# Optimization experiments

Measured on AMD Instinct MI355X. Metric: run time of the kernel, lower is better.

The kernel has to match this reference:

```python
import jax, jax.numpy as jnp
import numpy as np

B, C1, C2, D, NH, H, W = 2, 64, 256, 256, 8, 64, 64
HD = D // NH
EPS = 1e-5


def setup_inputs() -> dict:
    key = jax.random.key(0)
    ks = jax.random.split(key, 12)
    s = lambda fan_in: 1.0 / np.sqrt(fan_in)
    return {
        "F_lidar": jax.random.normal(ks[0], (B, C1, H, W), jnp.float32),
        "F_cam": jax.random.normal(ks[1], (B, C2, H, W), jnp.float32),
        "Wq": jax.random.normal(ks[2], (D, C1), jnp.float32) * s(C1),
        "Wk": jax.random.normal(ks[3], (D, C2), jnp.float32) * s(C2),
        "Wv": jax.random.normal(ks[4], (D, C2), jnp.float32) * s(C2),
        "Wo": jax.random.normal(ks[5], (D, D), jnp.float32) * s(D),
        "Wres": jax.random.normal(ks[6], (D, C1), jnp.float32) * s(C1),
        "g1": jnp.ones((D,), jnp.float32),
        "b1": jnp.zeros((D,), jnp.float32),
        "g2": jnp.ones((D,), jnp.float32),
        "b2": jnp.zeros((D,), jnp.float32),
        "W1": jax.random.normal(ks[7], (4 * D, D), jnp.float32) * s(D),
        "bf1": jnp.zeros((4 * D,), jnp.float32),
        "W2": jax.random.normal(ks[8], (D, 4 * D), jnp.float32) * s(4 * D),
        "bf2": jnp.zeros((D,), jnp.float32),
    }


def _layernorm(x, g, b):
    mu = jnp.mean(x, axis=-1, keepdims=True)
    var = jnp.mean(jnp.square(x - mu), axis=-1, keepdims=True)
    return (x - mu) * jax.lax.rsqrt(var + EPS) * g + b


def reference(F_lidar, F_cam, Wq, Wk, Wv, Wo, Wres, g1, b1, g2, b2, W1, bf1, W2, bf2):
    b, _, h, w = F_lidar.shape
    n = h * w
    # channels-last token views: (B, HW, C)
    xl = F_lidar.reshape(b, C1, n).transpose(0, 2, 1)
    xc = F_cam.reshape(b, C2, n).transpose(0, 2, 1)
    # 1x1 conv projections == per-token matmuls
    Q = jnp.einsum('bnc,dc->bnd', xl, Wq).reshape(b, n, NH, HD).transpose(0, 2, 1, 3)
    K = jnp.einsum('bnc,dc->bnd', xc, Wk).reshape(b, n, NH, HD).transpose(0, 2, 1, 3)
    V = jnp.einsum('bnc,dc->bnd', xc, Wv).reshape(b, n, NH, HD).transpose(0, 2, 1, 3)
    scale = HD ** -0.5
    scores = jnp.einsum('bhqd,bhkd->bhqk', Q, K) * scale  # (B,NH,HW,HW)
    attn = jax.nn.softmax(scores, axis=-1)
    out = jnp.einsum('bhqk,bhkd->bhqd', attn, V)
    out = out.transpose(0, 2, 1, 3).reshape(b, n, D)
    out = jnp.einsum('bnd,ed->bne', out, Wo)
    resid = jnp.einsum('bnc,dc->bnd', xl, Wres)
    x = _layernorm(resid + out, g1, b1)
    # FFN (dropout = identity in eval)
    hdn = jax.nn.relu(jnp.einsum('bnd,fd->bnf', x, W1) + bf1)
    ffn = jnp.einsum('bnf,df->bnd', hdn, W2) + bf2
    x = _layernorm(x + ffn, g2, b2)
    return x.transpose(0, 2, 1).reshape(b, D, h, w)
```

## Files before the change

kernel.cpp:

```cpp
#include <hip/hip_runtime.h>
#include <hip/hip_bf16.h>
#include <math.h>

#define NB 2
#define C1 64
#define C2 256
#define DD 256
#define NHH 8
#define HDD 32
#define NN 4096
#define FF 1024
#define MTOT (NB*NN)
#define KVB 128

typedef unsigned short u16;
typedef __attribute__((ext_vector_type(8))) short bf16x8;
typedef __attribute__((ext_vector_type(4))) float f32x4;
typedef __attribute__((ext_vector_type(4))) unsigned short us4;
typedef __attribute__((ext_vector_type(4))) unsigned int u32x4;

__device__ __forceinline__ u16 f2bf(float f) {
    union { float f; unsigned int i; } u; u.f = f;
    unsigned int r = u.i + 0x7FFFu + ((u.i >> 16) & 1u);
    return (u16)(r >> 16);
}

__device__ __forceinline__ unsigned cvt_pk_bf16(float a, float b) {
    unsigned r; asm("v_cvt_pk_bf16_f32 %0, %1, %2" : "=v"(r) : "v"(a), "v"(b)); return r;
}

__device__ __forceinline__ void glds16(const void* g, void* l) {
    __builtin_amdgcn_global_load_lds(
        (__attribute__((address_space(1))) void*)g,
        (__attribute__((address_space(3))) void*)l, 16, 0, 0);
}

__device__ __forceinline__ void tconv_body(const float* __restrict__ src,
    u16* __restrict__ dst, int C, int n0, int c0, int b, int t,
    float (*tile)[65])
{
#pragma unroll
    for (int i = 0; i < 4; ++i) {
        int cc = t + i * 256;
        int c = cc >> 4, off = (cc & 15) * 4;
        const float4 v = *(const float4*)&src[((size_t)b*C + c0 + c)*NN + n0 + off];
        tile[c][off+0] = v.x; tile[c][off+1] = v.y;
        tile[c][off+2] = v.z; tile[c][off+3] = v.w;
    }
    __syncthreads();
    const int n = t >> 2, cch = (t & 3) * 16;
    bf16x8 t0, t1;
#pragma unroll
    for (int i = 0; i < 8; ++i) ((u16*)&t0)[i] = f2bf(tile[cch + i][n]);
#pragma unroll
    for (int i = 0; i < 8; ++i) ((u16*)&t1)[i] = f2bf(tile[cch + 8 + i][n]);
    u16* dp = &dst[((size_t)b*NN + n0 + n)*C + c0 + cch];
    *(bf16x8*)&dp[0] = t0;
    *(bf16x8*)&dp[8] = t1;
}

__global__ __launch_bounds__(256) void prep(
    const float* __restrict__ Wq, const float* __restrict__ Wres,
    const float* __restrict__ Wk, const float* __restrict__ Wv,
    const float* __restrict__ Wo, const float* __restrict__ W1,
    const float* __restrict__ W2, u16* __restrict__ d,
    const float* __restrict__ F_lidar, const float* __restrict__ F_cam,
    u16* __restrict__ xl, u16* __restrict__ xc)
{
    __shared__ float tile[64][65];
    const int id = blockIdx.x, t = threadIdx.x;
    if (id < 736) {
        int i4 = (id * 256 + t) * 4;
        const float* s; int off;
        if      (i4 <  16384) { s = Wq;   off = i4; }
        else if (i4 <  32768) { s = Wres; off = i4 -  16384; }
        else if (i4 <  98304) { s = Wk;   off = i4 -  32768; }
        else if (i4 < 163840) { s = Wv;   off = i4 -  98304; }
        else if (i4 < 229376) { s = Wo;   off = i4 - 163840; }
        else if (i4 < 491520) { s = W1;   off = i4 - 229376; }
        else                  { s = W2;   off = i4 - 491520; }
        const float4 v = *(const float4*)&s[off];
        us4 o; o[0] = f2bf(v.x); o[1] = f2bf(v.y); o[2] = f2bf(v.z); o[3] = f2bf(v.w);
        *(us4*)&d[i4] = o;
    } else if (id < 864) {
        int l = id - 736;
        tconv_body(F_lidar, xl, C1, (l & 63)*64, 0, l >> 6, t, tile);
    } else {
        int l = id - 864;
        tconv_body(F_cam, xc, C2, (l & 63)*64, ((l >> 6) & 3)*64, l >> 8, t, tile);
    }
}

template<int MODE, int BM>
__device__ __forceinline__ void gemm_body(
    const u16* __restrict__ A, const u16* __restrict__ Bw,
    int N, int K,
    const float* __restrict__ bias, const float* __restrict__ add,
    float* __restrict__ outf, u16* __restrict__ outb, float scale,
    int bm, int bn, u16* lA, u16* lB)
{
    constexpr int MFR = BM / 32;
    constexpr int ASZ = BM * 32;
    const int t = threadIdx.x, lane = t & 63, wid = t >> 6;
    const int wr = (wid >> 1) * (BM/2), wc = (wid & 1) * 64;
    const int lrow = lane & 15, lk = (lane >> 4) * 8;
    const int arow = wid*(BM/4) + (lane >> 2);
    const int brow = wid*32 + (lane >> 2);
    const int soff = (lane & 3) * 8;
    const u16* aS = &A[(size_t)(bm + arow)*K + soff];
    const u16* bS = &Bw[(size_t)(bn + brow)*K + soff];
    const int lwA = wid*(BM/4)*32;
    const int lwB = wid*1024;
    f32x4 acc[MFR][4] = {};

    glds16(aS, &lA[lwA]);
    if (BM == 128) glds16(aS + (size_t)16*K, &lA[lwA + 512]);
    glds16(bS, &lB[lwB]);
    glds16(bS + (size_t)16*K, &lB[lwB + 512]);
    __syncthreads();

    const int nst = K >> 5;
    for (int st = 0; st < nst; ++st) {
        const int cur = st & 1;
        if (st < nst - 1) {
            const int k0 = (st + 1) * 32;
            const int nb = (cur ^ 1);
            glds16(aS + k0, &lA[nb*ASZ + lwA]);
            if (BM == 128) glds16(aS + (size_t)16*K + k0, &lA[nb*ASZ + lwA + 512]);
            glds16(bS + k0, &lB[nb*4096 + lwB]);
            glds16(bS + (size_t)16*K + k0, &lB[nb*4096 + lwB + 512]);
        }
        bf16x8 af[MFR], bfr[4];
#pragma unroll
        for (int mf = 0; mf < MFR; ++mf)
            af[mf] = *(const bf16x8*)&lA[cur*ASZ + (wr + mf*16 + lrow)*32 + lk];
#pragma unroll
        for (int nf = 0; nf < 4; ++nf)
            bfr[nf] = *(const bf16x8*)&lB[cur*4096 + (wc + nf*16 + lrow)*32 + lk];
#pragma unroll
        for (int mf = 0; mf < MFR; ++mf)
#pragma unroll
            for (int nf = 0; nf < 4; ++nf)
                acc[mf][nf] = __builtin_amdgcn_mfma_f32_16x16x32_bf16(af[mf], bfr[nf], acc[mf][nf], 0, 0, 0);
        __syncthreads();
    }
#pragma unroll
    for (int mf = 0; mf < MFR; ++mf) {
#pragma unroll
        for (int nf = 0; nf < 4; ++nf) {
#pragma unroll
            for (int j = 0; j < 4; ++j) {
                int row = bm + wr + mf*16 + (lane >> 4)*4 + j;
                int col = bn + wc + nf*16 + lrow;
                float v = acc[mf][nf][j];
                if (MODE == 1) {
                    float r = v + bias[col];
                    outb[(size_t)row*N + col] = f2bf(r > 0.f ? r : 0.f);
                } else if (MODE == 3) {
                    int b = row >> 12, n = row & 4095;
                    if (col < 256) {
                        int h = col >> 5, hd = col & 31;
                        int bh = b*NHH + h;
                        size_t idx = (((size_t)bh*256 + (n >> 4))*64
                                      + (hd >> 3)*16 + (n & 15))*8 + (hd & 7);
                        outb[idx] = f2bf(v);
                    } else {
                        int c = col - 256;
                        int h = c >> 5, hd = c & 31;
                        int hf = hd >> 4, d2 = hd & 15;
                        int bh = b*NHH + h;
                        int kb = n >> 5, kwb = n & 31;
                        int hp = kwb >> 4, gg = (kwb >> 2) & 3, r = kwb & 3;
                        size_t idx = ((((size_t)bh*128 + kb)*2 + hf)*64 + gg*16 + d2)*8
                                   + hp*4 + r;
                        ((u16*)outf)[idx] = f2bf(v);
                    }
                } else if (MODE == 4) {
                    int b = row >> 12, n = row & 4095;
                    if (col < 256) {
                        int h = col >> 5, hd = col & 31;
                        outb[(((size_t)b*NHH + h)*NN + n)*HDD + hd] = f2bf(v * scale);
                    } else {
                        outf[(size_t)row*DD + (col - 256)] = v;
                    }
                }
            }
        }
    }
}

template<int MODE, int BM>
__global__ __launch_bounds__(256) void gemm_bt(
    const u16* __restrict__ A, const u16* __restrict__ Bw,
    int N, int K, const float* __restrict__ bias, const float* __restrict__ add,
    float* __restrict__ outf, u16* __restrict__ outb, float scale)
{
    __shared__ u16 lA[2*BM*32];
    __shared__ u16 lB[2*4096];
    gemm_body<MODE, BM>(A, Bw, N, K, bias, add, outf, outb, scale,
                        blockIdx.x*BM, blockIdx.y*128, lA, lB);
}

__global__ __launch_bounds__(256) void qkv_gemm(
    const u16* __restrict__ xl, const u16* __restrict__ xc,
    const u16* __restrict__ WqRes, const u16* __restrict__ WkWv,
    float* __restrict__ resid, u16* __restrict__ Qb,
    u16* __restrict__ Kperm, u16* __restrict__ Vperm, float qscale)
{
    __shared__ u16 lA[2*128*32];
    __shared__ u16 lB[2*4096];
    int l = blockIdx.x;
    if (l < 256) {
        gemm_body<4, 128>(xl, WqRes, 512, 64, nullptr, nullptr, resid, Qb,
                          qscale, (l & 63)*128, (l >> 6)*128, lA, lB);
    } else {
        l -= 256;
        gemm_body<3, 128>(xc, WkWv, 512, 256, nullptr, nullptr,
                          (float*)Vperm, Kperm, 1.f, (l & 63)*128, (l >> 6)*128, lA, lB);
    }
}

template<int MODE>
__global__ __launch_bounds__(256) void gemm_ln(
    const u16* __restrict__ A, const u16* __restrict__ Bw, int K,
    const float* __restrict__ bias, const float* __restrict__ add,
    const float* __restrict__ g, const float* __restrict__ be,
    float* __restrict__ xf, u16* __restrict__ xb, float* __restrict__ out)
{
    __shared__ char smem[37888];
    u16* lA = (u16*)smem;
    u16* lB = (u16*)(smem + 4096);
    float (*epi)[257] = (float(*)[257])smem;

    const int bm = blockIdx.x * 32;
    const int t = threadIdx.x, lane = t & 63, wid = t >> 6;
    const int wc = wid * 64;
    const int lrow = lane & 15, g4 = lane >> 4, lk = g4 * 8;
    const int sr = lane >> 2, sc = (lane & 3) * 8;
    const u16* aS = &A[(size_t)(bm + wid*16 + sr)*K + sc];
    const u16* bS = &Bw[(size_t)(wid*64 + sr)*K + sc];
    f32x4 acc[2][4] = {};

    if (wid < 2) glds16(aS, &lA[wid*512]);
#pragma unroll
    for (int c = 0; c < 4; ++c)
        glds16(bS + (size_t)c*16*K, &lB[wid*2048 + c*512]);
    __syncthreads();

    const int nst = K >> 5;
    for (int st = 0; st < nst; ++st) {
        const int cur = st & 1;
        if (st < nst - 1) {
            const int k0 = (st + 1) * 32;
            const int nb = cur ^ 1;
            if (wid < 2) glds16(aS + k0, &lA[nb*1024 + wid*512]);
#pragma unroll
            for (int c = 0; c < 4; ++c)
                glds16(bS + (size_t)c*16*K + k0, &lB[nb*8192 + wid*2048 + c*512]);
        }
        bf16x8 af[2], bfr[4];
#pragma unroll
        for (int mf = 0; mf < 2; ++mf)
            af[mf] = *(const bf16x8*)&lA[cur*1024 + (mf*16 + lrow)*32 + lk];
#pragma unroll
        for (int nf = 0; nf < 4; ++nf)
            bfr[nf] = *(const bf16x8*)&lB[cur*8192 + (wc + nf*16 + lrow)*32 + lk];
#pragma unroll
        for (int mf = 0; mf < 2; ++mf)
#pragma unroll
            for (int nf = 0; nf < 4; ++nf)
                acc[mf][nf] = __builtin_amdgcn_mfma_f32_16x16x32_bf16(af[mf], bfr[nf], acc[mf][nf], 0, 0, 0);
        __syncthreads();
    }

#pragma unroll
    for (int mf = 0; mf < 2; ++mf)
#pragma unroll
        for (int nf = 0; nf < 4; ++nf)
#pragma unroll
            for (int j = 0; j < 4; ++j) {
                int rl = mf*16 + g4*4 + j;
                int col = wc + nf*16 + lrow;
                float v = acc[mf][nf][j];
                if (MODE == 0) v += add[(size_t)(bm + rl)*DD + col];
                else           v += bias[col] + add[(size_t)(bm + rl)*DD + col];
                epi[rl][col] = v;
            }
    __syncthreads();

#pragma unroll
    for (int r8 = 0; r8 < 8; ++r8) {
        int r = wid*8 + r8;
        const float4 v = *(const float4*)&epi[r][lane*4];
        float s1 = v.x + v.y + v.z + v.w;
        float s2 = v.x*v.x + v.y*v.y + v.z*v.z + v.w*v.w;
#pragma unroll
        for (int m = 1; m <= 32; m <<= 1) { s1 += __shfl_xor(s1, m); s2 += __shfl_xor(s2, m); }
        float mean = s1 * (1.f/DD);
        float var  = s2 * (1.f/DD) - mean*mean;
        float rstd = rsqrtf(var + 1e-5f);
        const float vv[4] = {v.x, v.y, v.z, v.w};
        if (MODE == 0) {
            float4 xo; us4 xo16;
#pragma unroll
            for (int i = 0; i < 4; ++i) {
                int d = lane*4 + i;
                float rr = (vv[i] - mean) * rstd * g[d] + be[d];
                ((float*)&xo)[i] = rr;
                xo16[i] = f2bf(rr);
            }
            *(float4*)&xf[(size_t)(bm + r)*DD + lane*4] = xo;
            *(us4*)&xb[(size_t)(bm + r)*DD + lane*4] = xo16;
        } else {
            float4 xo;
#pragma unroll
            for (int i = 0; i < 4; ++i) {
                int d = lane*4 + i;
                ((float*)&xo)[i] = (vv[i] - mean) * rstd * g[d] + be[d];
            }
            *(float4*)&epi[r][lane*4] = xo;
        }
    }
    if (MODE == 1) {
        __syncthreads();
        const int n = t & 31, dg = t >> 5;
        const int b = bm >> 12, n0 = bm & 4095;
#pragma unroll
        for (int dd = 0; dd < 32; ++dd) {
            int d = dd*8 + dg;
            out[((size_t)b*DD + d)*NN + n0 + n] = epi[n][d];
        }
    }
}

__global__ __launch_bounds__(256) void flash_attn(
    const u16* __restrict__ Qp, const u16* __restrict__ Kperm,
    const u16* __restrict__ Vperm, u16* __restrict__ Op)
{
    __shared__ u16 Kl[2][4096];
    __shared__ u16 Vl[2][4096];
    const int id = blockIdx.x;
    const int sw = (id & 7) * 128 + (id >> 3);
    const int qt = sw & 63;
    const int bh = sw >> 6;
    const size_t base = (size_t)bh * NN * HDD;
    const int t = threadIdx.x, lane = t & 63, w = t >> 6;
    const int q0 = qt * 64;
    const int lrow = lane & 15, g = lane >> 4;

    const bf16x8 qf = *(const bf16x8*)&Qp[base + (size_t)(q0 + w*16 + lrow)*HDD + g*8];

    const u16* kgw = &Kperm[(size_t)bh*131072 + w*1024 + lane*8];
    const u16* vgw = &Vperm[(size_t)bh*131072 + w*1024 + lane*8];
    const int lw = w * 1024;

    u32x4 onesw = {0x3F803F80u, 0x3F803F80u, 0x3F803F80u, 0x3F803F80u};
    const bf16x8 ones = *(bf16x8*)&onesw;

    glds16(kgw,       &Kl[0][lw]);
    glds16(kgw + 512, &Kl[0][lw + 512]);
    glds16(vgw,       &Vl[0][lw]);
    glds16(vgw + 512, &Vl[0][lw + 512]);

    f32x4 o[2] = {};
    f32x4 osum = {};
    __syncthreads();

#define FLASH_STEP(CUR, TT)                                                    \
    {                                                                          \
        if ((TT) < 31) {                                                       \
            const u16* kg = kgw + (size_t)((TT)+1)*4096;                       \
            const u16* vg = vgw + (size_t)((TT)+1)*4096;                       \
            glds16(kg,       &Kl[(CUR)^1][lw]);                                \
            glds16(kg + 512, &Kl[(CUR)^1][lw + 512]);                          \
            glds16(vg,       &Vl[(CUR)^1][lw]);                                \
            glds16(vg + 512, &Vl[(CUR)^1][lw + 512]);                          \
        }                                                                      \
        f32x4 s[8];                                                            \
        __builtin_amdgcn_s_setprio(1);                                         \
        _Pragma("unroll")                                                      \
        for (int nf = 0; nf < 8; ++nf) {                                       \
            bf16x8 kf = *(const bf16x8*)&Kl[(CUR)][nf*512 + lane*8];           \
            f32x4 z = {};                                                      \
            s[nf] = __builtin_amdgcn_mfma_f32_16x16x32_bf16(kf, qf, z, 0, 0, 0); \
        }                                                                      \
        __builtin_amdgcn_s_setprio(0);                                         \
        _Pragma("unroll")                                                      \
        for (int kk = 0; kk < 4; ++kk) {                                       \
            float p0[4], p1[4];                                                \
            _Pragma("unroll")                                                  \
            for (int jj = 0; jj < 4; ++jj) {                                   \
                p0[jj] = __builtin_amdgcn_exp2f(s[2*kk][jj]);                  \
                p1[jj] = __builtin_amdgcn_exp2f(s[2*kk+1][jj]);                 \
            }                                                                  \
            u32x4 paw;                                                         \
            paw[0] = cvt_pk_bf16(p0[0], p0[1]);                                \
            paw[1] = cvt_pk_bf16(p0[2], p0[3]);                                \
            paw[2] = cvt_pk_bf16(p1[0], p1[1]);                                \
            paw[3] = cvt_pk_bf16(p1[2], p1[3]);                                \
            bf16x8 pa = *(bf16x8*)&paw;                                        \
            __builtin_amdgcn_s_setprio(1);                                     \
            _Pragma("unroll")                                                  \
            for (int hf = 0; hf < 2; ++hf) {                                   \
                bf16x8 vf = *(const bf16x8*)&Vl[(CUR)][kk*1024 + hf*512 + lane*8]; \
                o[hf] = __builtin_amdgcn_mfma_f32_16x16x32_bf16(pa, vf, o[hf], 0, 0, 0); \
            }                                                                  \
            osum = __builtin_amdgcn_mfma_f32_16x16x32_bf16(pa, ones, osum, 0, 0, 0); \
            __builtin_amdgcn_s_setprio(0);                                     \
        }                                                                      \
        __syncthreads();                                                       \
    }

    for (int tt = 0; tt < 32; tt += 2) {
        FLASH_STEP(0, tt)
        FLASH_STEP(1, tt + 1)
    }
#undef FLASH_STEP

    const int b = bh >> 3, h = bh & 7;
#pragma unroll
    for (int hf = 0; hf < 2; ++hf)
#pragma unroll
        for (int r = 0; r < 4; ++r) {
            int q = q0 + w*16 + g*4 + r;
            int d = h*HDD + hf*16 + lrow;
            Op[((size_t)b*NN + q)*DD + d] = f2bf(o[hf][r] / osum[r]);
        }
}

extern "C" void kernel_launch(void* const* d_in, const int* in_sizes, int n_in,
                              void* d_out, int out_size, void* d_ws, size_t ws_size,
                              hipStream_t stream)
{
    const float* F_lidar = (const float*)d_in[0];
    const float* F_cam   = (const float*)d_in[1];
    const float* Wq  = (const float*)d_in[2];
    const float* Wk  = (const float*)d_in[3];
    const float* Wv  = (const float*)d_in[4];
    const float* Wo  = (const float*)d_in[5];
    const float* Wrs = (const float*)d_in[6];
    const float* g1  = (const float*)d_in[7];
    const float* b1  = (const float*)d_in[8];
    const float* g2  = (const float*)d_in[9];
    const float* b2  = (const float*)d_in[10];
    const float* W1  = (const float*)d_in[11];
    const float* bf1 = (const float*)d_in[12];
    const float* W2  = (const float*)d_in[13];
    const float* bf2 = (const float*)d_in[14];
    float* out = (float*)d_out;

    char* ws = (char*)d_ws;
    size_t cur = 0;
    auto carve = [&](size_t bytes) {
        size_t o = cur; cur += (bytes + 255) & ~(size_t)255; return (void*)(ws + o);
    };
    u16* wb    = (u16*)carve(753664u * 2);
    u16* xl    = (u16*)carve((size_t)MTOT * C1 * 2);
    u16* xc    = (u16*)carve((size_t)MTOT * C2 * 2);
    u16* Qb    = (u16*)carve((size_t)MTOT * DD * 2);
    u16* Kperm = (u16*)carve((size_t)MTOT * DD * 2);
    u16* Vperm = (u16*)carve((size_t)MTOT * DD * 2);
    float* resid = (float*)carve((size_t)MTOT * DD * 4);
    u16* attn  = (u16*)carve((size_t)MTOT * DD * 2);
    float* x   = (float*)carve((size_t)MTOT * DD * 4);
    u16* xb    = (u16*)carve((size_t)MTOT * DD * 2);
    u16* hdn   = (u16*)carve((size_t)MTOT * FF * 2);

    u16* WqRes = wb;
    u16* WkWv  = wb + 32768;
    u16* Wob   = wb + 163840;
    u16* W1b   = wb + 229376;
    u16* W2b   = wb + 491520;

    prep<<<1376, 256, 0, stream>>>(Wq, Wrs, Wk, Wv, Wo, W1, W2, wb,
                                   F_lidar, F_cam, xl, xc);

    const float qscale = 1.4426950408889634f / sqrtf((float)HDD);
    qkv_gemm<<<512, 256, 0, stream>>>(xl, xc, WqRes, WkWv,
                                      resid, Qb, Kperm, Vperm, qscale);

    flash_attn<<<1024, 256, 0, stream>>>(Qb, Kperm, Vperm, attn);

    gemm_ln<0><<<256, 256, 0, stream>>>(attn, Wob, DD,
        nullptr, resid, g1, b1, x, xb, nullptr);
    gemm_bt<1, 128><<<dim3(64, 8), 256, 0, stream>>>(xb, W1b, FF, DD,
        bf1, nullptr, nullptr, hdn, 1.f);
    gemm_ln<1><<<256, 256, 0, stream>>>(hdn, W2b, FF,
        bf2, x, g2, b2, nullptr, nullptr, out);
}
```

Measured before the change: 122.2 us.

## Move Wo/W1/W2 conversion into QKV kernel, drop fp32 LN1 output, remove setprio

The bf16 conversion of Wo, W1 and W2 moves out of the prep kernel and into extra blocks of the QKV GEMM launch, which shortens prep's critical path. The fp32 copy of the first LayerNorm output is no longer written, and the second LN kernel reads the bf16 copy for its residual. This cuts global traffic but rounds the residual to bf16, which costs some precision. The s_setprio hints are also removed from the flash attention inner loop.

```diff
diff --git a/kernel.cpp b/kernel.cpp
--- a/kernel.cpp
+++ b/kernel.cpp
@@ -11,7 +11,6 @@
 #define NN 4096
 #define FF 1024
 #define MTOT (NB*NN)
-#define KVB 128
 
 typedef unsigned short u16;
 typedef __attribute__((ext_vector_type(8))) short bf16x8;
@@ -23,6 +22,10 @@
     union { float f; unsigned int i; } u; u.f = f;
     unsigned int r = u.i + 0x7FFFu + ((u.i >> 16) & 1u);
     return (u16)(r >> 16);
+}
+
+__device__ __forceinline__ float bf2f(u16 x) {
+    union { unsigned i; float f; } u; u.i = ((unsigned)x) << 16; return u.f;
 }
 
 __device__ __forceinline__ unsigned cvt_pk_bf16(float a, float b) {
@@ -62,31 +65,27 @@
 __global__ __launch_bounds__(256) void prep(
     const float* __restrict__ Wq, const float* __restrict__ Wres,
     const float* __restrict__ Wk, const float* __restrict__ Wv,
-    const float* __restrict__ Wo, const float* __restrict__ W1,
-    const float* __restrict__ W2, u16* __restrict__ d,
+    u16* __restrict__ d,
     const float* __restrict__ F_lidar, const float* __restrict__ F_cam,
     u16* __restrict__ xl, u16* __restrict__ xc)
 {
     __shared__ float tile[64][65];
     const int id = blockIdx.x, t = threadIdx.x;
-    if (id < 736) {
+    if (id < 160) {
         int i4 = (id * 256 + t) * 4;
         const float* s; int off;
         if      (i4 <  16384) { s = Wq;   off = i4; }
         else if (i4 <  32768) { s = Wres; off = i4 -  16384; }
         else if (i4 <  98304) { s = Wk;   off = i4 -  32768; }
-        else if (i4 < 163840) { s = Wv;   off = i4 -  98304; }
-        else if (i4 < 229376) { s = Wo;   off = i4 - 163840; }
-        else if (i4 < 491520) { s = W1;   off = i4 - 229376; }
-        else                  { s = W2;   off = i4 - 491520; }
+        else                  { s = Wv;   off = i4 -  98304; }
         const float4 v = *(const float4*)&s[off];
         us4 o; o[0] = f2bf(v.x); o[1] = f2bf(v.y); o[2] = f2bf(v.z); o[3] = f2bf(v.w);
         *(us4*)&d[i4] = o;
-    } else if (id < 864) {
-        int l = id - 736;
+    } else if (id < 288) {
+        int l = id - 160;
         tconv_body(F_lidar, xl, C1, (l & 63)*64, 0, l >> 6, t, tile);
     } else {
-        int l = id - 864;
+        int l = id - 288;
         tconv_body(F_cam, xc, C2, (l & 63)*64, ((l >> 6) & 3)*64, l >> 8, t, tile);
     }
 }
@@ -95,7 +94,7 @@
 __device__ __forceinline__ void gemm_body(
     const u16* __restrict__ A, const u16* __restrict__ Bw,
     int N, int K,
-    const float* __restrict__ bias, const float* __restrict__ add,
+    const float* __restrict__ bias,
     float* __restrict__ outf, u16* __restrict__ outb, float scale,
     int bm, int bn, u16* lA, u16* lB)
 {
@@ -192,12 +191,12 @@
 template<int MODE, int BM>
 __global__ __launch_bounds__(256) void gemm_bt(
     const u16* __restrict__ A, const u16* __restrict__ Bw,
-    int N, int K, const float* __restrict__ bias, const float* __restrict__ add,
+    int N, int K, const float* __restrict__ bias,
     float* __restrict__ outf, u16* __restrict__ outb, float scale)
 {
     __shared__ u16 lA[2*BM*32];
     __shared__ u16 lB[2*4096];
-    gemm_body<MODE, BM>(A, Bw, N, K, bias, add, outf, outb, scale,
+    gemm_body<MODE, BM>(A, Bw, N, K, bias, outf, outb, scale,
                         blockIdx.x*BM, blockIdx.y*128, lA, lB);
 }
 
@@ -205,29 +204,41 @@
     const u16* __restrict__ xl, const u16* __restrict__ xc,
     const u16* __restrict__ WqRes, const u16* __restrict__ WkWv,
     float* __restrict__ resid, u16* __restrict__ Qb,
-    u16* __restrict__ Kperm, u16* __restrict__ Vperm, float qscale)
+    u16* __restrict__ Kperm, u16* __restrict__ Vperm, float qscale,
+    const float* __restrict__ Wo, const float* __restrict__ W1,
+    const float* __restrict__ W2, u16* __restrict__ wb)
 {
     __shared__ u16 lA[2*128*32];
     __shared__ u16 lB[2*4096];
     int l = blockIdx.x;
     if (l < 256) {
-        gemm_body<4, 128>(xl, WqRes, 512, 64, nullptr, nullptr, resid, Qb,
+        gemm_body<4, 128>(xl, WqRes, 512, 64, nullptr, resid, Qb,
                           qscale, (l & 63)*128, (l >> 6)*128, lA, lB);
+    } else if (l < 512) {
+        l -= 256;
+        gemm_body<3, 128>(xc, WkWv, 512, 256, nullptr, (float*)Vperm,
+                          Kperm, 1.f, (l & 63)*128, (l >> 6)*128, lA, lB);
     } else {
-        l -= 256;
-        gemm_body<3, 128>(xc, WkWv, 512, 256, nullptr, nullptr,
-                          (float*)Vperm, Kperm, 1.f, (l & 63)*128, (l >> 6)*128, lA, lB);
+        int i4 = ((l - 512) * 256 + threadIdx.x) * 4;
+        const float* s; int off;
+        if      (i4 <  65536) { s = Wo; off = i4; }
+        else if (i4 < 327680) { s = W1; off = i4 -  65536; }
+        else                  { s = W2; off = i4 - 327680; }
+        const float4 v = *(const float4*)&s[off];
+        us4 o; o[0] = f2bf(v.x); o[1] = f2bf(v.y); o[2] = f2bf(v.z); o[3] = f2bf(v.w);
+        *(us4*)&wb[163840 + i4] = o;
     }
 }
 
 template<int MODE>
 __global__ __launch_bounds__(256) void gemm_ln(
     const u16* __restrict__ A, const u16* __restrict__ Bw, int K,
-    const float* __restrict__ bias, const float* __restrict__ add,
+    const float* __restrict__ bias, const float* __restrict__ addf,
+    const u16* __restrict__ addb,
     const float* __restrict__ g, const float* __restrict__ be,
-    float* __restrict__ xf, u16* __restrict__ xb, float* __restrict__ out)
-{
-    __shared__ char smem[37888];
+    u16* __restrict__ xb, float* __restrict__ out)
+{
+    __shared__ __align__(16) char smem[37888];
     u16* lA = (u16*)smem;
     u16* lB = (u16*)(smem + 4096);
     float (*epi)[257] = (float(*)[257])smem;
@@ -282,8 +293,8 @@
                 int rl = mf*16 + g4*4 + j;
                 int col = wc + nf*16 + lrow;
                 float v = acc[mf][nf][j];
-                if (MODE == 0) v += add[(size_t)(bm + rl)*DD + col];
-                else           v += bias[col] + add[(size_t)(bm + rl)*DD + col];
+                if (MODE == 0) v += addf[(size_t)(bm + rl)*DD + col];
+                else           v += bias[col] + bf2f(addb[(size_t)(bm + rl)*DD + col]);
                 epi[rl][col] = v;
             }
     __syncthreads();
@@ -301,15 +312,12 @@
         float rstd = rsqrtf(var + 1e-5f);
         const float vv[4] = {v.x, v.y, v.z, v.w};
         if (MODE == 0) {
-            float4 xo; us4 xo16;
+            us4 xo16;
 #pragma unroll
             for (int i = 0; i < 4; ++i) {
                 int d = lane*4 + i;
-                float rr = (vv[i] - mean) * rstd * g[d] + be[d];
-                ((float*)&xo)[i] = rr;
-                xo16[i] = f2bf(rr);
+                xo16[i] = f2bf((vv[i] - mean) * rstd * g[d] + be[d]);
             }
-            *(float4*)&xf[(size_t)(bm + r)*DD + lane*4] = xo;
             *(us4*)&xb[(size_t)(bm + r)*DD + lane*4] = xo16;
         } else {
             float4 xo;
@@ -377,14 +385,12 @@
             glds16(vg + 512, &Vl[(CUR)^1][lw + 512]);                          \
         }                                                                      \
         f32x4 s[8];                                                            \
-        __builtin_amdgcn_s_setprio(1);                                         \
         _Pragma("unroll")                                                      \
         for (int nf = 0; nf < 8; ++nf) {                                       \
             bf16x8 kf = *(const bf16x8*)&Kl[(CUR)][nf*512 + lane*8];           \
             f32x4 z = {};                                                      \
             s[nf] = __builtin_amdgcn_mfma_f32_16x16x32_bf16(kf, qf, z, 0, 0, 0); \
         }                                                                      \
-        __builtin_amdgcn_s_setprio(0);                                         \
         _Pragma("unroll")                                                      \
         for (int kk = 0; kk < 4; ++kk) {                                       \
             float p0[4], p1[4];                                                \
@@ -399,14 +405,12 @@
             paw[2] = cvt_pk_bf16(p1[0], p1[1]);                                \
             paw[3] = cvt_pk_bf16(p1[2], p1[3]);                                \
             bf16x8 pa = *(bf16x8*)&paw;                                        \
-            __builtin_amdgcn_s_setprio(1);                                     \
             _Pragma("unroll")                                                  \
             for (int hf = 0; hf < 2; ++hf) {                                   \
                 bf16x8 vf = *(const bf16x8*)&Vl[(CUR)][kk*1024 + hf*512 + lane*8]; \
                 o[hf] = __builtin_amdgcn_mfma_f32_16x16x32_bf16(pa, vf, o[hf], 0, 0, 0); \
             }                                                                  \
             osum = __builtin_amdgcn_mfma_f32_16x16x32_bf16(pa, ones, osum, 0, 0, 0); \
-            __builtin_amdgcn_s_setprio(0);                                     \
         }                                                                      \
         __syncthreads();                                                       \
     }
@@ -462,7 +466,6 @@
     u16* Vperm = (u16*)carve((size_t)MTOT * DD * 2);
     float* resid = (float*)carve((size_t)MTOT * DD * 4);
     u16* attn  = (u16*)carve((size_t)MTOT * DD * 2);
-    float* x   = (float*)carve((size_t)MTOT * DD * 4);
     u16* xb    = (u16*)carve((size_t)MTOT * DD * 2);
     u16* hdn   = (u16*)carve((size_t)MTOT * FF * 2);
 
@@ -472,19 +475,19 @@
     u16* W1b   = wb + 229376;
     u16* W2b   = wb + 491520;
 
-    prep<<<1376, 256, 0, stream>>>(Wq, Wrs, Wk, Wv, Wo, W1, W2, wb,
-                                   F_lidar, F_cam, xl, xc);
+    prep<<<800, 256, 0, stream>>>(Wq, Wrs, Wk, Wv, wb, F_lidar, F_cam, xl, xc);
 
     const float qscale = 1.4426950408889634f / sqrtf((float)HDD);
-    qkv_gemm<<<512, 256, 0, stream>>>(xl, xc, WqRes, WkWv,
-                                      resid, Qb, Kperm, Vperm, qscale);
+    qkv_gemm<<<1088, 256, 0, stream>>>(xl, xc, WqRes, WkWv,
+                                       resid, Qb, Kperm, Vperm, qscale,
+                                       Wo, W1, W2, wb);
 
     flash_attn<<<1024, 256, 0, stream>>>(Qb, Kperm, Vperm, attn);
 
     gemm_ln<0><<<256, 256, 0, stream>>>(attn, Wob, DD,
-        nullptr, resid, g1, b1, x, xb, nullptr);
+        nullptr, resid, nullptr, g1, b1, xb, nullptr);
     gemm_bt<1, 128><<<dim3(64, 8), 256, 0, stream>>>(xb, W1b, FF, DD,
-        bf1, nullptr, nullptr, hdn, 1.f);
+        bf1, nullptr, hdn, 1.f);
     gemm_ln<1><<<256, 256, 0, stream>>>(hdn, W2b, FF,
-        bf2, x, g2, b2, nullptr, nullptr, out);
-}
+        bf2, nullptr, xb, g2, b2, nullptr, out);
+}
```

Measured after the change: 121.2 us. Within noise of the previous version (-0.8%).
